# Optimization experiments

Hardware: AMD Instinct MI355X
Metric: run time of the kernel (lower is better)

Reference implementation:

```python
import jax, jax.numpy as jnp
import numpy as np

NEG_INF = jnp.finfo(jnp.float32).min

def setup_inputs() -> dict:
    key = jax.random.key(0)
    k1, k2, k3, k4 = jax.random.split(key, 4)
    B, H, S, DK, DV = 2, 16, 2048, 64, 64
    Q = jax.random.normal(k1, (B, H, S, DK), dtype=jnp.float32)
    K = jax.random.normal(k2, (B, H, S, DK), dtype=jnp.float32)
    V = jax.random.normal(k3, (B, H, S, DV), dtype=jnp.float32)
    mask = jax.random.randint(k4, (B, 1, S, S), 0, 2, dtype=jnp.int32)
    return {"Q": Q, "K": K, "V": V, "mask": mask}

def reference(Q, K, V, mask):
    d_k = Q.shape[-1]
    # scores: [B, H, Sq, Sk]
    scores = jnp.einsum('bhqd,bhkd->bhqk', Q, K) / jnp.sqrt(jnp.float32(d_k))
    scores = jnp.where(mask == 0, NEG_INF, scores)
    attn_weights = jax.nn.softmax(scores, axis=-1)
    # dropout p=0.0 -> identity (eval-mode reference)
    output = jnp.einsum('bhqk,bhkv->bhqv', attn_weights, V)
    return (output, attn_weights)
```

## Files before the change

### kernel.cpp

```cpp
#include <hip/hip_runtime.h>


typedef __attribute__((ext_vector_type(4))) float f32x4;
typedef __attribute__((ext_vector_type(8))) short s16x8;
typedef __attribute__((ext_vector_type(4))) unsigned short u16x4;
typedef __attribute__((ext_vector_type(8))) unsigned short u16x8;
typedef __attribute__((ext_vector_type(4))) unsigned int u32x4;

#define S_LEN 2048
#define D_DIM 64
#define H_NUM 16
#define B_NUM 2
#define NT    32
#define SW    32
#define QSCALE 0.18033688011112042f

__device__ __forceinline__ int swz(int row, int colByte) {
  return row * 128 + (colByte ^ ((row & 7) << 4));
}

__device__ __forceinline__ unsigned short f2bf(float f) {
  unsigned int x = __builtin_bit_cast(unsigned int, f);
  x = (x + 0x7FFFu + ((x >> 16) & 1u)) >> 16;
  return (unsigned short)x;
}

__device__ __forceinline__ unsigned cvt_pk_bf16(float lo, float hi) {
  unsigned r;
  asm("v_cvt_pk_bf16_f32 %0, %1, %2" : "=v"(r) : "v"(lo), "v"(hi));
  return r;
}

__device__ __forceinline__ f32x4 mfma16(f32x4 acc, s16x8 a, s16x8 b) {
  return __builtin_amdgcn_mfma_f32_16x16x32_bf16(a, b, acc, 0, 0, 0);
}


__global__ __launch_bounds__(256) void prep_kernel(
    const float* __restrict__ Q, const float* __restrict__ K,
    const float* __restrict__ V, const int* __restrict__ m,
    u16x4* __restrict__ Q16, u16x4* __restrict__ K16,
    unsigned short* __restrict__ VT, unsigned long long* __restrict__ bits)
{
  const int blk = blockIdx.x;
  const int tid = threadIdx.x;

  if (blk < 1024) {
    __shared__ unsigned short t[64][72];
    const int bh = blk >> 5;
    const int st = blk & 31;
    const float* src = V + ((size_t)bh * S_LEN + st * 64) * D_DIM;
    const int r0 = tid >> 4;
    const int c  = (tid & 15) * 4;
#pragma unroll
    for (int i = 0; i < 4; ++i) {
      const int r = r0 + i * 16;
      float4 v = *(const float4*)(src + r * D_DIM + c);
      t[c + 0][r] = f2bf(v.x); t[c + 1][r] = f2bf(v.y);
      t[c + 2][r] = f2bf(v.z); t[c + 3][r] = f2bf(v.w);
    }
    __syncthreads();
#pragma unroll
    for (int i = 0; i < 4; ++i) {
      const int idx = tid + i * 256;
      const int d  = idx >> 4;
      const int t0 = (idx & 15) * 4;
      const int sp = ((t0 >> 5) & 1) * 32 + ((t0 & 7) >> 2) * 16 + ((t0 >> 3) & 3) * 4;
      u16x4 o = *(const u16x4*)&t[d][sp];
      *(u16x4*)(VT + ((size_t)bh * D_DIM + d) * S_LEN + st * 64 + t0) = o;
    }
  } else if (blk < 2048) {
    const int n4 = B_NUM * H_NUM * S_LEN * D_DIM / 4;
    const int step = 1024 * 256;
    for (int i = (blk - 1024) * 256 + tid; i < n4; i += step) {
      float4 q = ((const float4*)Q)[i];
      Q16[i] = u16x4{f2bf(q.x * QSCALE), f2bf(q.y * QSCALE),
                     f2bf(q.z * QSCALE), f2bf(q.w * QSCALE)};
      float4 k = ((const float4*)K)[i];
      K16[i] = u16x4{f2bf(k.x), f2bf(k.y), f2bf(k.z), f2bf(k.w)};
    }
  } else {
    const int total = B_NUM * S_LEN * S_LEN;
    const int step  = 1024 * 256;
    for (int i = (blk - 2048) * 256 + tid; i < total; i += step) {
      unsigned long long b = __ballot(m[i] != 0);
      if ((tid & 63) == 0) bits[i >> 6] = b;
    }
  }
}


__global__ __launch_bounds__(256) void attn_rowsum_kernel(
    const unsigned short* __restrict__ Q16, const unsigned short* __restrict__ K16,
    const unsigned long long* __restrict__ Mb, float* __restrict__ lpq)
{
  const int tid  = threadIdx.x;
  const int lane = tid & 63;
  const int wv   = tid >> 6;
  const int l15  = lane & 15;
  const int g4   = lane >> 4;

  const int wg = blockIdx.x;
  const int lg = (wg & 7) * 128 + (wg >> 3);
  const int qt = lg & 31;
  const int bh = lg >> 5;
  const int b  = bh >> 4;

  __shared__ __align__(16) char Kbuf[16384];

  const unsigned short* Qg16 = Q16 + ((size_t)bh * S_LEN + qt * 64 + wv * 16 + l15) * D_DIM + g4 * 8;
  const unsigned short* Kg16 = K16 + (size_t)bh * S_LEN * D_DIM;
  float* lpg = lpq + (size_t)bh * S_LEN + qt * 64;
  const unsigned long long* Mg = Mb + ((size_t)b * S_LEN + qt * 64) * SW;

  const s16x8 qa0 = *(const s16x8*)Qg16;
  const s16x8 qa1 = *(const s16x8*)(Qg16 + 32);

  float lps = 0.f;

  const int sr  = tid >> 3;
  const int ss  = tid & 7;
  const int ssb = ss * 16;

  {
    u16x8 k0 = *(const u16x8*)(Kg16 + (size_t)sr * D_DIM + ss * 8);
    u16x8 k1 = *(const u16x8*)(Kg16 + (size_t)(sr + 32) * D_DIM + ss * 8);
    *(u16x8*)(Kbuf + swz(sr, ssb))      = k0;
    *(u16x8*)(Kbuf + swz(sr + 32, ssb)) = k1;
  }
  __syncthreads();

  int cur = 0;
  for (int kt = 0; kt < NT; ++kt) {
    const int ktn = (kt + 1 < NT) ? kt + 1 : kt;
    u16x8 kr0 = *(const u16x8*)(Kg16 + (size_t)(ktn * 64 + sr) * D_DIM + ss * 8);
    u16x8 kr1 = *(const u16x8*)(Kg16 + (size_t)(ktn * 64 + sr + 32) * D_DIM + ss * 8);
    __builtin_amdgcn_sched_barrier(0);

    char* Kc = Kbuf + cur * 8192;
    const unsigned long long mw = Mg[(wv * 16 + l15) * SW + kt];

    f32x4 sacc[4];
#pragma unroll
    for (int i = 0; i < 4; ++i) sacc[i] = f32x4{0.f, 0.f, 0.f, 0.f};
#pragma unroll
    for (int ct = 0; ct < 4; ++ct) {
      s16x8 b0 = *(const s16x8*)(Kc + swz(ct * 16 + l15, g4 * 16));
      s16x8 b1 = *(const s16x8*)(Kc + swz(ct * 16 + l15, g4 * 16 + 64));
      sacc[ct] = mfma16(sacc[ct], b0, qa0);
      sacc[ct] = mfma16(sacc[ct], b1, qa1);
    }

#pragma unroll
    for (int ct = 0; ct < 4; ++ct) {
#pragma unroll
      for (int r = 0; r < 4; ++r) {
        float e = __builtin_amdgcn_exp2f(sacc[ct][r]);
        lps += ((mw >> (ct * 16 + g4 * 4 + r)) & 1ull) ? e : 0.f;
      }
    }

    char* Kn = Kbuf + (cur ^ 1) * 8192;
    *(u16x8*)(Kn + swz(sr, ssb))      = kr0;
    *(u16x8*)(Kn + swz(sr + 32, ssb)) = kr1;
    __syncthreads();
    cur ^= 1;
  }

  lps += __shfl_xor(lps, 16);
  lps += __shfl_xor(lps, 32);
  if (g4 == 0) lpg[wv * 16 + l15] = 1.0f / lps;
}


__global__ __launch_bounds__(512, 4) void attn_main_kernel(
    const unsigned short* __restrict__ Q16, const unsigned short* __restrict__ K16,
    const unsigned short* __restrict__ VT16, const unsigned long long* __restrict__ Mb,
    const float* __restrict__ lpq, float* __restrict__ Op, float* __restrict__ Wp)
{
  const int tid  = threadIdx.x;
  const int lane = tid & 63;
  const int wv   = tid >> 6;
  const int l15  = lane & 15;
  const int g4   = lane >> 4;
  const int wt   = wv & 3;

  const int wg = blockIdx.x;
  const int lg = (wg & 7) * 64 + (wg >> 3);
  const int tp = lg & 15;
  const int bh = lg >> 4;
  const int b  = bh >> 4;
  const int qt = tp * 2 + (wv >> 2);

  __shared__ __align__(16) char lds[32768];
  char* Kbuf = lds;
  char* Vbuf = lds + 16384;

  const unsigned short* Qg16 = Q16 + ((size_t)bh * S_LEN + qt * 64 + wt * 16 + l15) * D_DIM + g4 * 8;
  const unsigned short* Kg16 = K16 + (size_t)bh * S_LEN * D_DIM;
  const unsigned short* Vg   = VT16 + (size_t)bh * D_DIM * S_LEN;
  float* Og = Op + ((size_t)bh * S_LEN + qt * 64) * D_DIM;
  float* Wrow = Wp + ((size_t)bh * S_LEN + qt * 64 + wt * 16 + l15) * S_LEN;
  const unsigned long long* Mrow = Mb + ((size_t)b * S_LEN + qt * 64 + wt * 16 + l15) * SW;
  const float* lpg = lpq + (size_t)bh * S_LEN + qt * 64;

  const s16x8 qa0 = *(const s16x8*)Qg16;
  const s16x8 qa1 = *(const s16x8*)(Qg16 + 32);

  const float lpr = lpg[wt * 16 + l15];
  float lpn[4];
#pragma unroll
  for (int r = 0; r < 4; ++r) lpn[r] = lpg[wt * 16 + g4 * 4 + r];

  f32x4 oacc[4];
#pragma unroll
  for (int i = 0; i < 4; ++i) oacc[i] = f32x4{0.f, 0.f, 0.f, 0.f};

  const int sr  = tid >> 3;
  const int ss  = tid & 7;
  const int ssb = ss * 16;

  {
    u16x8 k0 = *(const u16x8*)(Kg16 + (size_t)sr * D_DIM + ss * 8);
    u16x8 v0 = *(const u16x8*)(Vg + (size_t)sr * S_LEN + ss * 8);
    *(u16x8*)(Kbuf + swz(sr, ssb)) = k0;
    *(u16x8*)(Vbuf + swz(sr, ssb)) = v0;
  }
  __syncthreads();

  int cur = 0;
  for (int kt = 0; kt < NT; ++kt) {
    const int ktn = (kt + 1 < NT) ? kt + 1 : kt;
    u16x8 kr = *(const u16x8*)(Kg16 + (size_t)(ktn * 64 + sr) * D_DIM + ss * 8);
    u16x8 vr = *(const u16x8*)(Vg + (size_t)sr * S_LEN + ktn * 64 + ss * 8);
    __builtin_amdgcn_sched_barrier(0);

    char* Kc = Kbuf + cur * 8192;
    char* Vc = Vbuf + cur * 8192;

    const unsigned long long mw = Mrow[kt];

    f32x4 sacc[4];
#pragma unroll
    for (int i = 0; i < 4; ++i) sacc[i] = f32x4{0.f, 0.f, 0.f, 0.f};
#pragma unroll
    for (int ct = 0; ct < 4; ++ct) {
      s16x8 b0 = *(const s16x8*)(Kc + swz(ct * 16 + l15, g4 * 16));
      s16x8 b1 = *(const s16x8*)(Kc + swz(ct * 16 + l15, g4 * 16 + 64));
      sacc[ct] = mfma16(sacc[ct], b0, qa0);
      sacc[ct] = mfma16(sacc[ct], b1, qa1);
    }

    unsigned pw[8];
#pragma unroll
    for (int ct = 0; ct < 4; ++ct) {
      float e0 = __builtin_amdgcn_exp2f(sacc[ct][0]);
      float e1 = __builtin_amdgcn_exp2f(sacc[ct][1]);
      float e2 = __builtin_amdgcn_exp2f(sacc[ct][2]);
      float e3 = __builtin_amdgcn_exp2f(sacc[ct][3]);
      e0 = ((mw >> (ct * 16 + g4 * 4 + 0)) & 1ull) ? e0 : 0.f;
      e1 = ((mw >> (ct * 16 + g4 * 4 + 1)) & 1ull) ? e1 : 0.f;
      e2 = ((mw >> (ct * 16 + g4 * 4 + 2)) & 1ull) ? e2 : 0.f;
      e3 = ((mw >> (ct * 16 + g4 * 4 + 3)) & 1ull) ? e3 : 0.f;
      f32x4 w = {e0 * lpr, e1 * lpr, e2 * lpr, e3 * lpr};
      __builtin_nontemporal_store(w,
          (f32x4*)(Wrow + (size_t)kt * 64 + ct * 16 + g4 * 4));
      pw[2 * ct]     = cvt_pk_bf16(e0, e1);
      pw[2 * ct + 1] = cvt_pk_bf16(e2, e3);
    }
    const s16x8 pa0 = __builtin_bit_cast(s16x8, u32x4{pw[0], pw[1], pw[2], pw[3]});
    const s16x8 pa1 = __builtin_bit_cast(s16x8, u32x4{pw[4], pw[5], pw[6], pw[7]});

#pragma unroll
    for (int ct = 0; ct < 4; ++ct) {
      s16x8 v0 = *(const s16x8*)(Vc + swz(ct * 16 + l15, g4 * 16));
      s16x8 v1 = *(const s16x8*)(Vc + swz(ct * 16 + l15, g4 * 16 + 64));
      oacc[ct] = mfma16(oacc[ct], pa0, v0);
      oacc[ct] = mfma16(oacc[ct], pa1, v1);
    }

    char* Kn = Kbuf + (cur ^ 1) * 8192;
    char* Vn = Vbuf + (cur ^ 1) * 8192;
    *(u16x8*)(Kn + swz(sr, ssb)) = kr;
    *(u16x8*)(Vn + swz(sr, ssb)) = vr;
    __syncthreads();
    cur ^= 1;
  }

#pragma unroll
  for (int ct = 0; ct < 4; ++ct)
#pragma unroll
    for (int r = 0; r < 4; ++r)
      Og[(size_t)(wt * 16 + g4 * 4 + r) * D_DIM + ct * 16 + l15] = oacc[ct][r] * lpn[r];
}


__global__ __launch_bounds__(256) void attn_fwd_kernel(
    const float* __restrict__ Qp, const float* __restrict__ Kp, const float* __restrict__ Vp,
    const int* __restrict__ Mi, float* __restrict__ Op, float* __restrict__ Wp)
{
  const int tid  = threadIdx.x;
  const int lane = tid & 63;
  const int wv   = tid >> 6;
  const int l15  = lane & 15;
  const int g4   = lane >> 4;

  const int wg = blockIdx.x;
  const int lg = (wg & 7) * 128 + (wg >> 3);
  const int qt = lg & 31;
  const int bh = lg >> 5;
  const int b  = bh >> 4;

  __shared__ __align__(16) char lds[32768];
  char* Qs  = lds;
  char* Ks  = lds + 8192;
  char* VTs = lds + 16384;
  char* Ps  = lds + 24576 + (wv << 11);

  const float* Qg = Qp + ((size_t)bh * S_LEN + qt * 64) * D_DIM;
  const float* Kg = Kp + (size_t)bh * S_LEN * D_DIM;
  const float* Vg = Vp + (size_t)bh * S_LEN * D_DIM;
  float* Og = Op + ((size_t)bh * S_LEN + qt * 64) * D_DIM;
  float* Wg = Wp + ((size_t)bh * S_LEN + qt * 64) * S_LEN;
  const int* Mig = Mi + ((size_t)b * S_LEN + qt * 64) * S_LEN;

  {
    const int r0 = tid >> 4;
    const int c  = (tid & 15) * 4;
#pragma unroll
    for (int i = 0; i < 4; ++i) {
      const int r = r0 + i * 16;
      float4 v = *(const float4*)(Qg + r * D_DIM + c);
      ushort4 p; p.x = f2bf(v.x); p.y = f2bf(v.y); p.z = f2bf(v.z); p.w = f2bf(v.w);
      *(ushort4*)(Qs + swz(r, c * 2)) = p;
    }
  }
  __syncthreads();
  const s16x8 qa0 = *(const s16x8*)(Qs + swz(wv * 16 + l15, g4 * 16));
  const s16x8 qa1 = *(const s16x8*)(Qs + swz(wv * 16 + l15, g4 * 16 + 64));

  f32x4 oacc[4];
#pragma unroll
  for (int i = 0; i < 4; ++i) oacc[i] = f32x4{0.f, 0.f, 0.f, 0.f};
  float lp[4] = {0.f, 0.f, 0.f, 0.f};

  const int qrow = wv * 16 + g4 * 4;

  for (int kt = 0; kt < NT; ++kt) {
    __syncthreads();
    {
      const int r0 = tid >> 4;
      const int c  = (tid & 15) * 4;
      const float* Kt = Kg + kt * 64 * D_DIM;
#pragma unroll
      for (int i = 0; i < 4; ++i) {
        const int r = r0 + i * 16;
        float4 v = *(const float4*)(Kt + r * D_DIM + c);
        ushort4 p; p.x = f2bf(v.x); p.y = f2bf(v.y); p.z = f2bf(v.z); p.w = f2bf(v.w);
        *(ushort4*)(Ks + swz(r, c * 2)) = p;
      }
      const float* Vt = Vg + kt * 64 * D_DIM;
#pragma unroll
      for (int i = 0; i < 2; ++i) {
        const int rr = (tid >> 4) * 2 + i * 32;
        float4 a  = *(const float4*)(Vt + rr * D_DIM + c);
        float4 bq = *(const float4*)(Vt + (rr + 1) * D_DIM + c);
        const float av[4] = {a.x, a.y, a.z, a.w};
        const float bv[4] = {bq.x, bq.y, bq.z, bq.w};
#pragma unroll
        for (int j = 0; j < 4; ++j) {
          unsigned pk = (unsigned)f2bf(av[j]) | ((unsigned)f2bf(bv[j]) << 16);
          *(unsigned*)(VTs + swz(c + j, rr * 2)) = pk;
        }
      }
    }
    __syncthreads();

    f32x4 sacc[4];
#pragma unroll
    for (int i = 0; i < 4; ++i) sacc[i] = f32x4{0.f, 0.f, 0.f, 0.f};
#pragma unroll
    for (int ct = 0; ct < 4; ++ct) {
      s16x8 b0 = *(const s16x8*)(Ks + swz(ct * 16 + l15, g4 * 16));
      s16x8 b1 = *(const s16x8*)(Ks + swz(ct * 16 + l15, g4 * 16 + 64));
      sacc[ct] = mfma16(sacc[ct], qa0, b0);
      sacc[ct] = mfma16(sacc[ct], qa1, b1);
    }

#pragma unroll
    for (int ct = 0; ct < 4; ++ct) {
#pragma unroll
      for (int r = 0; r < 4; ++r) {
        float e = __expf(sacc[ct][r] * 0.125f);
        bool keep = Mig[(size_t)(qrow + r) * S_LEN + kt * 64 + ct * 16 + l15] != 0;
        e = keep ? e : 0.f;
        lp[r] += e;
        *(unsigned short*)(Ps + swz(g4 * 4 + r, (ct * 16 + l15) * 2)) = f2bf(e);
      }
    }
    asm volatile("s_waitcnt lgkmcnt(0)" ::: "memory");
    __builtin_amdgcn_sched_barrier(0);

    const s16x8 pa0 = *(const s16x8*)(Ps + swz(l15, g4 * 16));
    const s16x8 pa1 = *(const s16x8*)(Ps + swz(l15, g4 * 16 + 64));
#pragma unroll
    for (int ct = 0; ct < 4; ++ct) {
      s16x8 v0 = *(const s16x8*)(VTs + swz(ct * 16 + l15, g4 * 16));
      s16x8 v1 = *(const s16x8*)(VTs + swz(ct * 16 + l15, g4 * 16 + 64));
      oacc[ct] = mfma16(oacc[ct], pa0, v0);
      oacc[ct] = mfma16(oacc[ct], pa1, v1);
    }
  }

#pragma unroll
  for (int r = 0; r < 4; ++r) {
    float v = lp[r];
    v += __shfl_xor(v, 1);
    v += __shfl_xor(v, 2);
    v += __shfl_xor(v, 4);
    v += __shfl_xor(v, 8);
    lp[r] = 1.0f / v;
  }

#pragma unroll
  for (int ct = 0; ct < 4; ++ct)
#pragma unroll
    for (int r = 0; r < 4; ++r)
      Og[(size_t)(qrow + r) * D_DIM + ct * 16 + l15] = oacc[ct][r] * lp[r];

  for (int kt = 0; kt < NT; ++kt) {
    __syncthreads();
    {
      const int r0 = tid >> 4;
      const int c  = (tid & 15) * 4;
      const float* Kt = Kg + kt * 64 * D_DIM;
#pragma unroll
      for (int i = 0; i < 4; ++i) {
        const int r = r0 + i * 16;
        float4 v = *(const float4*)(Kt + r * D_DIM + c);
        ushort4 p; p.x = f2bf(v.x); p.y = f2bf(v.y); p.z = f2bf(v.z); p.w = f2bf(v.w);
        *(ushort4*)(Ks + swz(r, c * 2)) = p;
      }
    }
    __syncthreads();

    f32x4 sacc[4];
#pragma unroll
    for (int i = 0; i < 4; ++i) sacc[i] = f32x4{0.f, 0.f, 0.f, 0.f};
#pragma unroll
    for (int ct = 0; ct < 4; ++ct) {
      s16x8 b0 = *(const s16x8*)(Ks + swz(ct * 16 + l15, g4 * 16));
      s16x8 b1 = *(const s16x8*)(Ks + swz(ct * 16 + l15, g4 * 16 + 64));
      sacc[ct] = mfma16(sacc[ct], qa0, b0);
      sacc[ct] = mfma16(sacc[ct], qa1, b1);
    }

#pragma unroll
    for (int ct = 0; ct < 4; ++ct) {
#pragma unroll
      for (int r = 0; r < 4; ++r) {
        float e = __expf(sacc[ct][r] * 0.125f);
        bool keep = Mig[(size_t)(qrow + r) * S_LEN + kt * 64 + ct * 16 + l15] != 0;
        e = keep ? e : 0.f;
        __builtin_nontemporal_store(e * lp[r],
            Wg + (size_t)(qrow + r) * S_LEN + kt * 64 + ct * 16 + l15);
      }
    }
  }
}

extern "C" void kernel_launch(void* const* d_in, const int* in_sizes, int n_in,
                              void* d_out, int out_size, void* d_ws, size_t ws_size,
                              hipStream_t stream) {
  (void)in_sizes; (void)n_in; (void)out_size;
  const float* Q   = (const float*)d_in[0];
  const float* K   = (const float*)d_in[1];
  const float* V   = (const float*)d_in[2];
  const int* mask  = (const int*)d_in[3];
  float* Out = (float*)d_out;
  float* W   = Out + (size_t)B_NUM * H_NUM * S_LEN * D_DIM;

  const size_t bits_bytes = (size_t)(B_NUM * S_LEN * S_LEN / 64) * 8;
  const size_t t16_bytes  = (size_t)B_NUM * H_NUM * S_LEN * D_DIM * 2;
  const size_t lp_bytes   = (size_t)B_NUM * H_NUM * S_LEN * 4;
  unsigned long long* bits = (unsigned long long*)d_ws;

  if (ws_size >= bits_bytes + 3 * t16_bytes + lp_bytes) {
    unsigned short* Q16 = (unsigned short*)((char*)d_ws + bits_bytes);
    unsigned short* K16 = Q16 + t16_bytes / 2;
    unsigned short* VT  = K16 + t16_bytes / 2;
    float* lpq = (float*)((char*)d_ws + bits_bytes + 3 * t16_bytes);
    prep_kernel<<<3072, 256, 0, stream>>>(Q, K, V, mask,
                                          (u16x4*)Q16, (u16x4*)K16, VT, bits);
    attn_rowsum_kernel<<<1024, 256, 0, stream>>>(Q16, K16, bits, lpq);
    attn_main_kernel<<<512, 512, 0, stream>>>(Q16, K16, VT, bits, lpq, Out, W);
  } else {
    attn_fwd_kernel<<<1024, 256, 0, stream>>>(Q, K, V, mask, Out, W);
  }
}
```

Before: 241.0 us.

## Split attention main kernel over key halves with separate partial-output reduction

The main attention kernel now splits the key range in two, so the grid doubles and each block processes half the key tiles. Each block writes an unnormalized partial output to a workspace buffer. A new reduce kernel sums the two partials and applies the precomputed reciprocal row sum. The goal is more parallelism and better load balance for the write-heavy main kernel. The cost is extra global traffic for the partial outputs and one more launch, and a larger workspace requirement that may push execution onto the slow fallback path.

```diff
diff --git a/kernel.cpp b/kernel.cpp
--- a/kernel.cpp
+++ b/kernel.cpp
@@ -176,7 +176,7 @@
 __global__ __launch_bounds__(512, 4) void attn_main_kernel(
     const unsigned short* __restrict__ Q16, const unsigned short* __restrict__ K16,
     const unsigned short* __restrict__ VT16, const unsigned long long* __restrict__ Mb,
-    const float* __restrict__ lpq, float* __restrict__ Op, float* __restrict__ Wp)
+    const float* __restrict__ lpq, float* __restrict__ pO, float* __restrict__ Wp)
 {
   const int tid  = threadIdx.x;
   const int lane = tid & 63;
@@ -186,9 +186,10 @@
   const int wt   = wv & 3;
 
   const int wg = blockIdx.x;
-  const int lg = (wg & 7) * 64 + (wg >> 3);
-  const int tp = lg & 15;
-  const int bh = lg >> 4;
+  const int lg = (wg & 7) * 128 + (wg >> 3);
+  const int kc = lg & 1;
+  const int tp = (lg >> 1) & 15;
+  const int bh = lg >> 5;
   const int b  = bh >> 4;
   const int qt = tp * 2 + (wv >> 2);
 
@@ -199,7 +200,8 @@
   const unsigned short* Qg16 = Q16 + ((size_t)bh * S_LEN + qt * 64 + wt * 16 + l15) * D_DIM + g4 * 8;
   const unsigned short* Kg16 = K16 + (size_t)bh * S_LEN * D_DIM;
   const unsigned short* Vg   = VT16 + (size_t)bh * D_DIM * S_LEN;
-  float* Og = Op + ((size_t)bh * S_LEN + qt * 64) * D_DIM;
+  float* pOg = pO + (size_t)kc * (B_NUM * H_NUM * S_LEN * D_DIM)
+                  + ((size_t)bh * S_LEN + qt * 64) * D_DIM;
   float* Wrow = Wp + ((size_t)bh * S_LEN + qt * 64 + wt * 16 + l15) * S_LEN;
   const unsigned long long* Mrow = Mb + ((size_t)b * S_LEN + qt * 64 + wt * 16 + l15) * SW;
   const float* lpg = lpq + (size_t)bh * S_LEN + qt * 64;
@@ -208,9 +210,6 @@
   const s16x8 qa1 = *(const s16x8*)(Qg16 + 32);
 
   const float lpr = lpg[wt * 16 + l15];
-  float lpn[4];
-#pragma unroll
-  for (int r = 0; r < 4; ++r) lpn[r] = lpg[wt * 16 + g4 * 4 + r];
 
   f32x4 oacc[4];
 #pragma unroll
@@ -220,17 +219,20 @@
   const int ss  = tid & 7;
   const int ssb = ss * 16;
 
+  const int kt0 = kc * (NT / 2);
+  const int kt1 = kt0 + (NT / 2);
+
   {
-    u16x8 k0 = *(const u16x8*)(Kg16 + (size_t)sr * D_DIM + ss * 8);
-    u16x8 v0 = *(const u16x8*)(Vg + (size_t)sr * S_LEN + ss * 8);
+    u16x8 k0 = *(const u16x8*)(Kg16 + (size_t)(kt0 * 64 + sr) * D_DIM + ss * 8);
+    u16x8 v0 = *(const u16x8*)(Vg + (size_t)sr * S_LEN + kt0 * 64 + ss * 8);
     *(u16x8*)(Kbuf + swz(sr, ssb)) = k0;
     *(u16x8*)(Vbuf + swz(sr, ssb)) = v0;
   }
   __syncthreads();
 
   int cur = 0;
-  for (int kt = 0; kt < NT; ++kt) {
-    const int ktn = (kt + 1 < NT) ? kt + 1 : kt;
+  for (int kt = kt0; kt < kt1; ++kt) {
+    const int ktn = (kt + 1 < kt1) ? kt + 1 : kt;
     u16x8 kr = *(const u16x8*)(Kg16 + (size_t)(ktn * 64 + sr) * D_DIM + ss * 8);
     u16x8 vr = *(const u16x8*)(Vg + (size_t)sr * S_LEN + ktn * 64 + ss * 8);
     __builtin_amdgcn_sched_barrier(0);
@@ -291,7 +293,26 @@
   for (int ct = 0; ct < 4; ++ct)
 #pragma unroll
     for (int r = 0; r < 4; ++r)
-      Og[(size_t)(wt * 16 + g4 * 4 + r) * D_DIM + ct * 16 + l15] = oacc[ct][r] * lpn[r];
+      pOg[(size_t)(wt * 16 + g4 * 4 + r) * D_DIM + ct * 16 + l15] = oacc[ct][r];
+}
+
+
+__global__ __launch_bounds__(256) void o_reduce_kernel(
+    const float* __restrict__ pO, const float* __restrict__ lpq,
+    float* __restrict__ Op)
+{
+  const int n4 = B_NUM * H_NUM * S_LEN * D_DIM / 4;
+  const int step = gridDim.x * blockDim.x;
+  const f32x4* p0 = (const f32x4*)pO;
+  const f32x4* p1 = p0 + n4;
+  for (int i = blockIdx.x * blockDim.x + threadIdx.x; i < n4; i += step) {
+    f32x4 a = p0[i];
+    f32x4 bq = p1[i];
+    const float s = lpq[i >> 4];
+    f32x4 o = {(a[0] + bq[0]) * s, (a[1] + bq[1]) * s,
+               (a[2] + bq[2]) * s, (a[3] + bq[3]) * s};
+    __builtin_nontemporal_store(o, (f32x4*)&((f32x4*)Op)[i]);
+  }
 }
 
 
@@ -483,17 +504,22 @@
   const size_t bits_bytes = (size_t)(B_NUM * S_LEN * S_LEN / 64) * 8;
   const size_t t16_bytes  = (size_t)B_NUM * H_NUM * S_LEN * D_DIM * 2;
   const size_t lp_bytes   = (size_t)B_NUM * H_NUM * S_LEN * 4;
+  const size_t pO_bytes   = (size_t)2 * B_NUM * H_NUM * S_LEN * D_DIM * 4;
   unsigned long long* bits = (unsigned long long*)d_ws;
 
-  if (ws_size >= bits_bytes + 3 * t16_bytes + lp_bytes) {
+  if (ws_size >= bits_bytes + 3 * t16_bytes + lp_bytes + pO_bytes) {
     unsigned short* Q16 = (unsigned short*)((char*)d_ws + bits_bytes);
     unsigned short* K16 = Q16 + t16_bytes / 2;
     unsigned short* VT  = K16 + t16_bytes / 2;
     float* lpq = (float*)((char*)d_ws + bits_bytes + 3 * t16_bytes);
+    float* pO  = (float*)((char*)d_ws + bits_bytes + 3 * t16_bytes + lp_bytes);
     prep_kernel<<<3072, 256, 0, stream>>>(Q, K, V, mask,
                                           (u16x4*)Q16, (u16x4*)K16, VT, bits);
     attn_rowsum_kernel<<<1024, 256, 0, stream>>>(Q16, K16, bits, lpq);
-    attn_main_kernel<<<512, 512, 0, stream>>>(Q16, K16, VT, bits, lpq, Out, W);
+    attn_main_kernel<<<1024, 512, 0, stream>>>(Q16, K16, VT, bits, lpq, pO, W);
+    o_reduce_kernel<<<2048, 256, 0, stream>>>(pO, lpq, Out);
+  } else if (ws_size >= bits_bytes + 3 * t16_bytes + lp_bytes) {
+    attn_fwd_kernel<<<1024, 256, 0, stream>>>(Q, K, V, mask, Out, W);
   } else {
     attn_fwd_kernel<<<1024, 256, 0, stream>>>(Q, K, V, mask, Out, W);
   }
```

After: 253.3 us. +5.1%, slower.
